# Optimization experiments

Measured on AMD Instinct MI355X. Metric: run time of the kernel, lower is better.

The kernel has to match this reference:

```python
import jax, jax.numpy as jnp
import numpy as np

BLOCK_SIZE = 64
NUM_STEPS = 3
# pad_type='post', init_type='ones', attention_mask=None


def setup_inputs() -> dict:
    key = jax.random.key(0)
    k1, k2, k3 = jax.random.split(key, 3)
    B, H, S, D = 4, 16, 4096, 64
    return {
        "query": jax.random.normal(k1, (B, H, S, D), dtype=jnp.float32),
        "key": jax.random.normal(k2, (B, H, S, D), dtype=jnp.float32),
        "value": jax.random.normal(k3, (B, H, S, D), dtype=jnp.float32),
    }


def _soba_monarch(query, key, value):
    B, H, S, D = query.shape
    bs = BLOCK_SIZE
    nb = -(-S // bs)                 # ceil(S / bs)
    pad = nb * bs - S                # post padding amount
    q = query / (D ** 0.5)

    pad_cfg = ((0, 0), (0, 0), (0, pad), (0, 0))
    Qb = jnp.pad(q, pad_cfg).reshape(B, H, nb, bs, D)      # (l j) v -> l j v
    Kb = jnp.pad(key, pad_cfg).reshape(B, H, nb, bs, D)    # (k i) v -> k i v

    # validity of positions in the padded sequence (post-pad)
    pos_valid = (jnp.arange(nb * bs) < S).reshape(nb, bs)  # [block, within]
    # left factor shape (..., j, l, k): rows of the flattened (l j) axis
    left_mask = jnp.broadcast_to(pos_valid.T[:, :, None], (bs, nb, nb))      # j l k
    # right factor shape (..., k, j, i): columns of the flattened (k i) axis
    right_mask = jnp.broadcast_to(pos_valid[:, None, :], (nb, bs, bs))       # k j i

    NEG = jnp.finfo(q.dtype).min
    # init_type = 'ones'
    left = jnp.broadcast_to(
        jnp.where(left_mask, 1.0 / nb, 0.0), (B, H, bs, nb, nb)
    ).astype(q.dtype)

    for _ in range(NUM_STEPS):
        # beta[k,j,i] = sum_{l,v} left[j,l,k] Q[l,j,v] K[k,i,v]
        beta = jnp.einsum('bhjlk,bhljv,bhkiv->bhkji', left, Qb, Kb, optimize=True)
        tau = jnp.swapaxes(jnp.sum(left, axis=-2), -1, -2)[..., None]        # bhkj1
        tau_zero = jnp.isclose(tau, 0.0)
        tau_safe = jnp.where(tau_zero, 1.0, tau)
        logits_r = jnp.where(right_mask & ~tau_zero, beta / tau_safe, NEG)
        right = jax.nn.softmax(logits_r, axis=-1)
        right = jnp.where(right_mask, right, 0.0)

        # alpha[j,1,k] = sum_i right[k,j,i] log right[k,j,i]  (xlogy)
        r_safe = jnp.where(right > 0, right, 1.0)
        alpha = jnp.sum(right * jnp.log(r_safe), axis=-1)                    # bhkj
        alpha = jnp.swapaxes(alpha, -1, -2)[..., None, :]                    # bhj1k

        beta2 = jnp.einsum('bhkji,bhljv,bhkiv->bhjlk', right, Qb, Kb, optimize=True)
        left = jax.nn.softmax(jnp.where(left_mask, beta2 - alpha, NEG), axis=-1)
        left = jnp.where(left_mask, left, 0.0)

    # multiply: z = L (R V)
    Vb = jnp.pad(value, pad_cfg).reshape(B, H, nb, bs, D)                    # k i v
    Y = jnp.einsum('bhkji,bhkiv->bhkjv', right, Vb)
    Z = jnp.einsum('bhjlk,bhkjv->bhljv', left, Y)
    z = Z.reshape(B, H, nb * bs, D)
    return z[..., :S, :]


def reference(query, key, value):
    return _soba_monarch(query, key, value)
```

## Files before the change

kernel.cpp:

```cpp
#include <hip/hip_runtime.h>


namespace {

typedef __attribute__((ext_vector_type(8))) short short8v;
typedef __attribute__((ext_vector_type(4))) float f32x4;

constexpr int HEADS = 64;
constexpr size_t HEADQ = 262144;
constexpr size_t MATF  = (size_t)HEADS * 262144;

#define MFMA(ACC, A, B) ACC = __builtin_amdgcn_mfma_f32_16x16x32_bf16(A, B, ACC, 0, 0, 0)
#define LD8(arr, row, g8) (*(const short8v*)((arr) + (row) * 72 + (g8) * 8))

__device__ __forceinline__ float rmax16(float m) {
    m = fmaxf(m, __shfl_xor(m, 1));
    m = fmaxf(m, __shfl_xor(m, 2));
    m = fmaxf(m, __shfl_xor(m, 4));
    m = fmaxf(m, __shfl_xor(m, 8));
    return m;
}
__device__ __forceinline__ float rsum16(float s) {
    s += __shfl_xor(s, 1);
    s += __shfl_xor(s, 2);
    s += __shfl_xor(s, 4);
    s += __shfl_xor(s, 8);
    return s;
}

__device__ __forceinline__ void bfsplit(float x, ushort& h, ushort& l) {
    uint u = __float_as_uint(x);
    uint hi = (u + 0x7FFFu + ((u >> 16) & 1u)) & 0xFFFF0000u;
    h = (ushort)(hi >> 16);
    l = (ushort)(__float_as_uint(x - __uint_as_float(hi)) >> 16);
}
__device__ __forceinline__ uint packbf(float x) {
    uint u = __float_as_uint(x);
    uint hi = (u + 0x7FFFu + ((u >> 16) & 1u)) & 0xFFFF0000u;
    return hi | (__float_as_uint(x - __uint_as_float(hi)) >> 16);
}

struct Frag16 { short8v h0, h1, l0, l1; };

__device__ __forceinline__ Frag16 split_load(const float* __restrict__ p, float s) {
    Frag16 f;
    #pragma unroll
    for (int q = 0; q < 4; ++q) {
        float4 a = *(const float4*)(p + 4 * q);
        float v[4] = {a.x * s, a.y * s, a.z * s, a.w * s};
        #pragma unroll
        for (int e = 0; e < 4; ++e) {
            ushort hh, ll; bfsplit(v[e], hh, ll);
            const int i = 4 * q + e;
            if (i < 8) { f.h0[i] = (short)hh; f.l0[i] = (short)ll; }
            else       { f.h1[i - 8] = (short)hh; f.l1[i - 8] = (short)ll; }
        }
    }
    return f;
}
__device__ __forceinline__ Frag16 unpack_load(const uint* __restrict__ p) {
    Frag16 f;
    #pragma unroll
    for (int q = 0; q < 2; ++q) {
        uint4 a = *(const uint4*)(p + 8 * q);
        uint4 b = *(const uint4*)(p + 8 * q + 4);
        uint vv[8] = {a.x, a.y, a.z, a.w, b.x, b.y, b.z, b.w};
        short8v h, l;
        #pragma unroll
        for (int e = 0; e < 8; ++e) {
            h[e] = (short)(vv[e] >> 16);
            l[e] = (short)(vv[e] & 0xFFFFu);
        }
        if (q == 0) { f.h0 = h; f.l0 = l; } else { f.h1 = h; f.l1 = l; }
    }
    return f;
}
__device__ __forceinline__ void store_rows(ushort* H, ushort* L, int r, int c0,
                                           const Frag16& f) {
    *(short8v*)(H + r * 72 + c0)     = f.h0;
    *(short8v*)(H + r * 72 + c0 + 8) = f.h1;
    *(short8v*)(L + r * 72 + c0)     = f.l0;
    *(short8v*)(L + r * 72 + c0 + 8) = f.l1;
}
__device__ __forceinline__ void scatter_tr(ushort* H, ushort* L, int r, int c0,
                                           const Frag16& f) {
    #pragma unroll
    for (int e = 0; e < 8; ++e) {
        H[(c0 + e) * 72 + r] = (ushort)f.h0[e];
        L[(c0 + e) * 72 + r] = (ushort)f.l0[e];
    }
    #pragma unroll
    for (int e = 0; e < 8; ++e) {
        H[(c0 + 8 + e) * 72 + r] = (ushort)f.h1[e];
        L[(c0 + 8 + e) * 72 + r] = (ushort)f.l1[e];
    }
}

__device__ __forceinline__ void mmstep(const ushort* AH, const ushort* AL,
                                       const ushort* BH, const ushort* BL,
                                       int w, int lo4, int hi4, f32x4 acc[4]) {
    #pragma unroll
    for (int ks = 0; ks < 2; ++ks) {
        short8v ah = LD8(AH, 16 * w + lo4, hi4 + 4 * ks);
        short8v al = LD8(AL, 16 * w + lo4, hi4 + 4 * ks);
        #pragma unroll
        for (int t = 0; t < 4; ++t) {
            short8v bh = LD8(BH, 16 * t + lo4, hi4 + 4 * ks);
            short8v bl = LD8(BL, 16 * t + lo4, hi4 + 4 * ks);
            MFMA(acc[t], ah, bh); MFMA(acc[t], ah, bl); MFMA(acc[t], al, bh);
        }
    }
}

__global__ __launch_bounds__(256) void kmean_kernel(const float* __restrict__ Q,
                                                    uint* __restrict__ M) {
    const int wg = blockIdx.x;
    const int h  = wg >> 4;
    const int j  = ((wg & 15) << 2) + (threadIdx.x >> 6);
    const int v  = threadIdx.x & 63;
    const float* base = Q + (size_t)h * HEADQ + (size_t)j * 64 + v;
    float acc = 0.f;
    #pragma unroll
    for (int l = 0; l < 64; ++l) acc += base[(size_t)l * 4096];
    M[((size_t)h * 64 + j) * 64 + v] = packbf(acc * (1.0f / 512.0f));
}

template<int FIRST, int LAST>
__global__ __launch_bounds__(256, 4) void bc_kernel(
    const uint*  __restrict__ Gsrc,
    const float* __restrict__ Kmat,
    const float* __restrict__ Vmat,
    const float* __restrict__ tauIn,
    uint*  __restrict__ HmOut,
    float* __restrict__ alphaOut,
    uint*  __restrict__ Yout)
{
    __shared__ __align__(16) ushort SM[18432];
    ushort* Ah = SM;          ushort* Al = SM + 4608;
    ushort* Bh = SM + 9216;   ushort* Bl = SM + 13824;

    const int wg = blockIdx.x, h = wg >> 6, k = wg & 63;
    const int tid = threadIdx.x, r = tid & 63, c0 = (tid >> 6) << 4;
    const int w = tid >> 6, lo4 = tid & 15, hi4 = (tid >> 4) & 3;

    {
        const uint* gp = FIRST ? Gsrc + ((size_t)h * 64 + r) * 64 + c0
                               : Gsrc + ((size_t)h * 64 + r) * 4096 + (size_t)k * 64 + c0;
        store_rows(Ah, Al, r, c0, unpack_load(gp));
    }
    Frag16 fk = split_load(Kmat + (size_t)h * HEADQ + (size_t)k * 4096 + r * 64 + c0, 1.f);
    store_rows(Bh, Bl, r, c0, fk);
    Frag16 fv;
    if (LAST)
        fv = split_load(Vmat + (size_t)h * HEADQ + (size_t)k * 4096 + r * 64 + c0, 1.f);
    float tvv[4];
    #pragma unroll
    for (int rr = 0; rr < 4; ++rr)
        tvv[rr] = FIRST ? 1.f : tauIn[((size_t)h * 64 + 16 * w + 4 * hi4 + rr) * 64 + k];
    __syncthreads();

    f32x4 acc[4] = {};
    mmstep(Ah, Al, Bh, Bl, w, lo4, hi4, acc);
    __syncthreads();

    #pragma unroll
    for (int rr = 0; rr < 4; ++rr) {
        const int j = 16 * w + 4 * hi4 + rr;
        const bool tz = !(tvv[rr] > 1e-8f);
        const float tvi = tz ? 1.f : 1.f / tvv[rr];
        float lg[4];
        #pragma unroll
        for (int t = 0; t < 4; ++t) lg[t] = acc[t][rr] * tvi;
        float m = rmax16(fmaxf(fmaxf(lg[0], lg[1]), fmaxf(lg[2], lg[3])));
        float e[4], s = 0.f;
        #pragma unroll
        for (int t = 0; t < 4; ++t) { e[t] = __expf(lg[t] - m); s += e[t]; }
        s = rsum16(s);
        const float inv = 1.f / s;
        float ap = 0.f;
        #pragma unroll
        for (int t = 0; t < 4; ++t) {
            const float rv = tz ? (1.f / 64.f) : e[t] * inv;
            ap += (rv > 0.f) ? rv * __logf(rv) : 0.f;
            ushort hh, ll; bfsplit(rv, hh, ll);
            Ah[j * 72 + 16 * t + lo4] = hh;
            Al[j * 72 + 16 * t + lo4] = ll;
        }
        ap = rsum16(ap);
        if (lo4 == 0) alphaOut[((size_t)h * 64 + k) * 64 + j] = ap;
    }
    scatter_tr(Bh, Bl, r, c0, fk);
    __syncthreads();

    f32x4 acc2[4] = {};
    mmstep(Ah, Al, Bh, Bl, w, lo4, hi4, acc2);
    f32x4 acc3[4] = {};
    if (LAST) {
        __syncthreads();
        scatter_tr(Bh, Bl, r, c0, fv);
        __syncthreads();
        mmstep(Ah, Al, Bh, Bl, w, lo4, hi4, acc3);
    }

    #pragma unroll
    for (int rr = 0; rr < 4; ++rr) {
        const int j = 16 * w + 4 * hi4 + rr;
        const size_t ob = ((size_t)h * 64 + k) * 4096 + (size_t)j * 64;
        #pragma unroll
        for (int t = 0; t < 4; ++t) {
            HmOut[ob + 16 * t + lo4] = packbf(acc2[t][rr]);
            if (LAST) Yout[ob + 16 * t + lo4] = packbf(acc3[t][rr]);
        }
    }
}

template<int LAST>
__global__ __launch_bounds__(256, 4) void da_kernel(
    const float* __restrict__ Q,
    const uint*  __restrict__ HmIn,
    const float* __restrict__ alphaIn,
    const uint*  __restrict__ Yin,
    uint*  __restrict__ Gout,
    float* __restrict__ tauOut,
    float* __restrict__ Zout)
{
    __shared__ __align__(16) ushort SM[18432];
    ushort* Ah = SM;          ushort* Al = SM + 4608;
    ushort* Bh = SM + 9216;   ushort* Bl = SM + 13824;

    const int wg = blockIdx.x, h = wg >> 6, j = wg & 63;
    const int tid = threadIdx.x, r = tid & 63, c0 = (tid >> 6) << 4;
    const int w = tid >> 6, lo4 = tid & 15, hi4 = (tid >> 4) & 3;

    Frag16 fq = split_load(Q + (size_t)h * HEADQ + (size_t)r * 4096 + (size_t)j * 64 + c0,
                           0.125f);
    store_rows(Ah, Al, r, c0, fq);
    {
        store_rows(Bh, Bl, r, c0,
                   unpack_load(HmIn + ((size_t)h * 64 + r) * 4096 + (size_t)j * 64 + c0));
    }
    Frag16 fy;
    if (LAST)
        fy = unpack_load(Yin + ((size_t)h * 64 + r) * 4096 + (size_t)j * 64 + c0);
    float av[4];
    #pragma unroll
    for (int t = 0; t < 4; ++t)
        av[t] = alphaIn[((size_t)h * 64 + 16 * t + lo4) * 64 + j];
    __syncthreads();

    f32x4 acc[4] = {};
    mmstep(Ah, Al, Bh, Bl, w, lo4, hi4, acc);
    __syncthreads();

    #pragma unroll
    for (int rr = 0; rr < 4; ++rr) {
        const int l = 16 * w + 4 * hi4 + rr;
        float lg[4];
        #pragma unroll
        for (int t = 0; t < 4; ++t) lg[t] = acc[t][rr] - av[t];
        float m = rmax16(fmaxf(fmaxf(lg[0], lg[1]), fmaxf(lg[2], lg[3])));
        float e[4], s = 0.f;
        #pragma unroll
        for (int t = 0; t < 4; ++t) { e[t] = __expf(lg[t] - m); s += e[t]; }
        s = rsum16(s);
        const float inv = 1.f / s;
        #pragma unroll
        for (int t = 0; t < 4; ++t) {
            const float lv = e[t] * inv;
            ushort hh, ll; bfsplit(lv, hh, ll);
            if (!LAST) { Bh[(16 * t + lo4) * 72 + l] = hh; Bl[(16 * t + lo4) * 72 + l] = ll; }
            else       { Bh[l * 72 + 16 * t + lo4] = hh; Bl[l * 72 + 16 * t + lo4] = ll; }
        }
    }
    if (!LAST) scatter_tr(Ah, Al, r, c0, fq);
    else       scatter_tr(Ah, Al, r, c0, fy);
    __syncthreads();

    if (!LAST) {
        f32x4 acc2[4] = {};
        f32x4 tacc = {};
        short8v onesb;
        #pragma unroll
        for (int e2 = 0; e2 < 8; ++e2) onesb[e2] = (lo4 == 0) ? (short)0x3F80 : (short)0;
        #pragma unroll
        for (int ks = 0; ks < 2; ++ks) {
            short8v ah = LD8(Bh, 16 * w + lo4, hi4 + 4 * ks);
            short8v al = LD8(Bl, 16 * w + lo4, hi4 + 4 * ks);
            MFMA(tacc, ah, onesb); MFMA(tacc, al, onesb);
            #pragma unroll
            for (int t = 0; t < 4; ++t) {
                short8v bh = LD8(Ah, 16 * t + lo4, hi4 + 4 * ks);
                short8v bl = LD8(Al, 16 * t + lo4, hi4 + 4 * ks);
                MFMA(acc2[t], ah, bh); MFMA(acc2[t], ah, bl); MFMA(acc2[t], al, bh);
            }
        }
        #pragma unroll
        for (int rr = 0; rr < 4; ++rr) {
            const int kq = 16 * w + 4 * hi4 + rr;
            if (lo4 == 0) tauOut[((size_t)h * 64 + j) * 64 + kq] = tacc[rr];
            const size_t gb = ((size_t)h * 64 + j) * 4096 + (size_t)kq * 64;
            #pragma unroll
            for (int t = 0; t < 4; ++t) Gout[gb + 16 * t + lo4] = packbf(acc2[t][rr]);
        }
    } else {
        f32x4 acc2[4] = {};
        #pragma unroll
        for (int ks = 0; ks < 2; ++ks) {
            short8v ah = LD8(Bh, 16 * w + lo4, hi4 + 4 * ks);
            short8v al = LD8(Bl, 16 * w + lo4, hi4 + 4 * ks);
            #pragma unroll
            for (int t = 0; t < 4; ++t) {
                short8v bh = LD8(Ah, 16 * t + lo4, hi4 + 4 * ks);
                short8v bl = LD8(Al, 16 * t + lo4, hi4 + 4 * ks);
                MFMA(acc2[t], ah, bh); MFMA(acc2[t], ah, bl); MFMA(acc2[t], al, bh);
            }
        }
        #pragma unroll
        for (int rr = 0; rr < 4; ++rr) {
            const int l = 16 * w + 4 * hi4 + rr;
            const size_t zb = (size_t)h * HEADQ + (size_t)l * 4096 + (size_t)j * 64;
            #pragma unroll
            for (int t = 0; t < 4; ++t) Zout[zb + 16 * t + lo4] = acc2[t][rr];
        }
    }
}

}

extern "C" void kernel_launch(void* const* d_in, const int* in_sizes, int n_in,
                              void* d_out, int out_size, void* d_ws, size_t ws_size,
                              hipStream_t stream) {
    const float* Q = (const float*)d_in[0];
    const float* K = (const float*)d_in[1];
    const float* V = (const float*)d_in[2];
    float* out = (float*)d_out;

    char* ws = (char*)d_ws;
    const size_t MB = 1024 * 1024;
    uint*  G   = (uint*)(ws);
    uint*  Hm  = (uint*)(ws + 64 * MB);
    uint*  M   = (uint*)(ws + 128 * MB);
    float* al  = (float*)(ws + 129 * MB);
    float* tau = (float*)(ws + 130 * MB);

    const bool bigws = ws_size >= (size_t)195 * MB;
    uint*  Ybuf = bigws ? (uint*)(ws + 131 * MB) : (uint*)out;
    float* Zdst = bigws ? out : (float*)G;

    dim3 blk(256), grid(HEADS * 64);

    kmean_kernel<<<dim3(1024), blk, 0, stream>>>(Q, M);
    bc_kernel<1, 0><<<grid, blk, 0, stream>>>(M, K, nullptr, nullptr, Hm, al, nullptr);
    da_kernel<0>   <<<grid, blk, 0, stream>>>(Q, Hm, al, nullptr, G, tau, nullptr);
    bc_kernel<0, 0><<<grid, blk, 0, stream>>>(G, K, nullptr, tau, Hm, al, nullptr);
    da_kernel<0>   <<<grid, blk, 0, stream>>>(Q, Hm, al, nullptr, G, tau, nullptr);
    bc_kernel<0, 1><<<grid, blk, 0, stream>>>(G, K, V, tau, Hm, al, Ybuf);
    da_kernel<1>   <<<grid, blk, 0, stream>>>(Q, Hm, al, Ybuf, nullptr, nullptr, Zdst);
    if (!bigws)
        hipMemcpyAsync(d_out, Zdst, MATF * sizeof(float), hipMemcpyDeviceToDevice, stream);
}
```

Before: 328.9 us.

## Process two blocks per workgroup with register prefetch of next block's inputs

Both bc and da kernels now handle two consecutive k/j blocks per workgroup, halving the grid. While computing the current block, they prefetch the next block's raw G/K/tau or Q/Hm/alpha data into registers so global latency overlaps the MFMA work. The alpha and tau buffers are transposed so per-block reads become contiguous. The trade-offs are fewer workgroups in flight, more registers, and extra barriers per iteration.

```diff
diff --git a/kernel.cpp b/kernel.cpp
--- a/kernel.cpp
+++ b/kernel.cpp
@@ -40,38 +40,42 @@
     return hi | (__float_as_uint(x - __uint_as_float(hi)) >> 16);
 }
 
+struct RawU  { uint4 a, b, c, d; };
+struct RawF  { float4 a, b, c, d; };
 struct Frag16 { short8v h0, h1, l0, l1; };
 
-__device__ __forceinline__ Frag16 split_load(const float* __restrict__ p, float s) {
+__device__ __forceinline__ RawU loadU(const uint* __restrict__ p) {
+    RawU r;
+    r.a = *(const uint4*)(p);      r.b = *(const uint4*)(p + 4);
+    r.c = *(const uint4*)(p + 8);  r.d = *(const uint4*)(p + 12);
+    return r;
+}
+__device__ __forceinline__ RawF loadF(const float* __restrict__ p) {
+    RawF r;
+    r.a = *(const float4*)(p);     r.b = *(const float4*)(p + 4);
+    r.c = *(const float4*)(p + 8); r.d = *(const float4*)(p + 12);
+    return r;
+}
+__device__ __forceinline__ Frag16 unpackR(const RawU& r) {
+    uint vv[16] = {r.a.x, r.a.y, r.a.z, r.a.w, r.b.x, r.b.y, r.b.z, r.b.w,
+                   r.c.x, r.c.y, r.c.z, r.c.w, r.d.x, r.d.y, r.d.z, r.d.w};
     Frag16 f;
     #pragma unroll
-    for (int q = 0; q < 4; ++q) {
-        float4 a = *(const float4*)(p + 4 * q);
-        float v[4] = {a.x * s, a.y * s, a.z * s, a.w * s};
-        #pragma unroll
-        for (int e = 0; e < 4; ++e) {
-            ushort hh, ll; bfsplit(v[e], hh, ll);
-            const int i = 4 * q + e;
-            if (i < 8) { f.h0[i] = (short)hh; f.l0[i] = (short)ll; }
-            else       { f.h1[i - 8] = (short)hh; f.l1[i - 8] = (short)ll; }
-        }
+    for (int e = 0; e < 8; ++e) {
+        f.h0[e] = (short)(vv[e] >> 16);      f.l0[e] = (short)(vv[e] & 0xFFFFu);
+        f.h1[e] = (short)(vv[e + 8] >> 16);  f.l1[e] = (short)(vv[e + 8] & 0xFFFFu);
     }
     return f;
 }
-__device__ __forceinline__ Frag16 unpack_load(const uint* __restrict__ p) {
+__device__ __forceinline__ Frag16 splitR(const RawF& r, float s) {
+    float vv[16] = {r.a.x*s, r.a.y*s, r.a.z*s, r.a.w*s, r.b.x*s, r.b.y*s, r.b.z*s, r.b.w*s,
+                    r.c.x*s, r.c.y*s, r.c.z*s, r.c.w*s, r.d.x*s, r.d.y*s, r.d.z*s, r.d.w*s};
     Frag16 f;
     #pragma unroll
-    for (int q = 0; q < 2; ++q) {
-        uint4 a = *(const uint4*)(p + 8 * q);
-        uint4 b = *(const uint4*)(p + 8 * q + 4);
-        uint vv[8] = {a.x, a.y, a.z, a.w, b.x, b.y, b.z, b.w};
-        short8v h, l;
-        #pragma unroll
-        for (int e = 0; e < 8; ++e) {
-            h[e] = (short)(vv[e] >> 16);
-            l[e] = (short)(vv[e] & 0xFFFFu);
-        }
-        if (q == 0) { f.h0 = h; f.l0 = l; } else { f.h1 = h; f.l1 = l; }
+    for (int e = 0; e < 16; ++e) {
+        ushort hh, ll; bfsplit(vv[e], hh, ll);
+        if (e < 8) { f.h0[e] = (short)hh; f.l0[e] = (short)ll; }
+        else       { f.h1[e - 8] = (short)hh; f.l1[e - 8] = (short)ll; }
     }
     return f;
 }
@@ -139,78 +143,109 @@
     ushort* Ah = SM;          ushort* Al = SM + 4608;
     ushort* Bh = SM + 9216;   ushort* Bl = SM + 13824;
 
-    const int wg = blockIdx.x, h = wg >> 6, k = wg & 63;
+    const int wg = blockIdx.x, h = wg >> 5, k0 = (wg & 31) << 1;
     const int tid = threadIdx.x, r = tid & 63, c0 = (tid >> 6) << 4;
     const int w = tid >> 6, lo4 = tid & 15, hi4 = (tid >> 4) & 3;
 
-    {
-        const uint* gp = FIRST ? Gsrc + ((size_t)h * 64 + r) * 64 + c0
-                               : Gsrc + ((size_t)h * 64 + r) * 4096 + (size_t)k * 64 + c0;
-        store_rows(Ah, Al, r, c0, unpack_load(gp));
-    }
-    Frag16 fk = split_load(Kmat + (size_t)h * HEADQ + (size_t)k * 4096 + r * 64 + c0, 1.f);
-    store_rows(Bh, Bl, r, c0, fk);
-    Frag16 fv;
-    if (LAST)
-        fv = split_load(Vmat + (size_t)h * HEADQ + (size_t)k * 4096 + r * 64 + c0, 1.f);
-    float tvv[4];
-    #pragma unroll
-    for (int rr = 0; rr < 4; ++rr)
-        tvv[rr] = FIRST ? 1.f : tauIn[((size_t)h * 64 + 16 * w + 4 * hi4 + rr) * 64 + k];
-    __syncthreads();
-
-    f32x4 acc[4] = {};
-    mmstep(Ah, Al, Bh, Bl, w, lo4, hi4, acc);
-    __syncthreads();
-
-    #pragma unroll
-    for (int rr = 0; rr < 4; ++rr) {
-        const int j = 16 * w + 4 * hi4 + rr;
-        const bool tz = !(tvv[rr] > 1e-8f);
-        const float tvi = tz ? 1.f : 1.f / tvv[rr];
-        float lg[4];
+    const uint*  gB = Gsrc + (FIRST ? ((size_t)h * 64 + r) * 64 + c0
+                                    : ((size_t)h * 64 + r) * 4096 + c0);
+    const float* kB = Kmat + (size_t)h * HEADQ + (size_t)r * 64 + c0;
+
+    RawU gcur = loadU(FIRST ? gB : gB + (size_t)k0 * 64);
+    RawF kcur = loadF(kB + (size_t)k0 * 4096);
+    float tcur0, tcur1, tcur2, tcur3;
+    if (!FIRST) {
+        const float* tp = tauIn + ((size_t)h * 64 + k0) * 64 + 16 * w + 4 * hi4;
+        tcur0 = tp[0]; tcur1 = tp[1]; tcur2 = tp[2]; tcur3 = tp[3];
+    } else { tcur0 = tcur1 = tcur2 = tcur3 = 1.f; }
+
+    #pragma unroll
+    for (int t = 0; t < 2; ++t) {
+        const int k = k0 + t;
+
+        store_rows(Ah, Al, r, c0, unpackR(gcur));
+        Frag16 fk = splitR(kcur, 1.f);
+        store_rows(Bh, Bl, r, c0, fk);
+
+        RawU gnext; RawF knext;
+        float tn0 = 1.f, tn1 = 1.f, tn2 = 1.f, tn3 = 1.f;
+        if (t == 0) {
+            gnext = loadU(FIRST ? gB : gB + (size_t)(k + 1) * 64);
+            knext = loadF(kB + (size_t)(k + 1) * 4096);
+            if (!FIRST) {
+                const float* tp = tauIn + ((size_t)h * 64 + k + 1) * 64 + 16 * w + 4 * hi4;
+                tn0 = tp[0]; tn1 = tp[1]; tn2 = tp[2]; tn3 = tp[3];
+            }
+        }
+        __syncthreads();
+
+        f32x4 acc[4] = {};
+        mmstep(Ah, Al, Bh, Bl, w, lo4, hi4, acc);
+        __syncthreads();
+
+        RawF vraw;
+        if (LAST)
+            vraw = loadF(Vmat + (size_t)h * HEADQ + (size_t)k * 4096 + r * 64 + c0);
+
+        const float tvv[4] = {tcur0, tcur1, tcur2, tcur3};
         #pragma unroll
-        for (int t = 0; t < 4; ++t) lg[t] = acc[t][rr] * tvi;
-        float m = rmax16(fmaxf(fmaxf(lg[0], lg[1]), fmaxf(lg[2], lg[3])));
-        float e[4], s = 0.f;
+        for (int rr = 0; rr < 4; ++rr) {
+            const int j = 16 * w + 4 * hi4 + rr;
+            const bool tz = !(tvv[rr] > 1e-8f);
+            const float tvi = tz ? 1.f : 1.f / tvv[rr];
+            float lg[4];
+            #pragma unroll
+            for (int tt = 0; tt < 4; ++tt) lg[tt] = acc[tt][rr] * tvi;
+            float m = rmax16(fmaxf(fmaxf(lg[0], lg[1]), fmaxf(lg[2], lg[3])));
+            float e[4], s = 0.f;
+            #pragma unroll
+            for (int tt = 0; tt < 4; ++tt) { e[tt] = __expf(lg[tt] - m); s += e[tt]; }
+            s = rsum16(s);
+            const float inv = 1.f / s;
+            float ap = 0.f;
+            #pragma unroll
+            for (int tt = 0; tt < 4; ++tt) {
+                const float rv = tz ? (1.f / 64.f) : e[tt] * inv;
+                ap += (rv > 0.f) ? rv * __logf(rv) : 0.f;
+                ushort hh, ll; bfsplit(rv, hh, ll);
+                Ah[j * 72 + 16 * tt + lo4] = hh;
+                Al[j * 72 + 16 * tt + lo4] = ll;
+            }
+            ap = rsum16(ap);
+            if (lo4 == 0) alphaOut[((size_t)h * 64 + j) * 64 + k] = ap;
+        }
+        scatter_tr(Bh, Bl, r, c0, fk);
+        __syncthreads();
+
+        f32x4 acc2[4] = {};
+        mmstep(Ah, Al, Bh, Bl, w, lo4, hi4, acc2);
         #pragma unroll
-        for (int t = 0; t < 4; ++t) { e[t] = __expf(lg[t] - m); s += e[t]; }
-        s = rsum16(s);
-        const float inv = 1.f / s;
-        float ap = 0.f;
-        #pragma unroll
-        for (int t = 0; t < 4; ++t) {
-            const float rv = tz ? (1.f / 64.f) : e[t] * inv;
-            ap += (rv > 0.f) ? rv * __logf(rv) : 0.f;
-            ushort hh, ll; bfsplit(rv, hh, ll);
-            Ah[j * 72 + 16 * t + lo4] = hh;
-            Al[j * 72 + 16 * t + lo4] = ll;
-        }
-        ap = rsum16(ap);
-        if (lo4 == 0) alphaOut[((size_t)h * 64 + k) * 64 + j] = ap;
-    }
-    scatter_tr(Bh, Bl, r, c0, fk);
-    __syncthreads();
-
-    f32x4 acc2[4] = {};
-    mmstep(Ah, Al, Bh, Bl, w, lo4, hi4, acc2);
-    f32x4 acc3[4] = {};
-    if (LAST) {
-        __syncthreads();
-        scatter_tr(Bh, Bl, r, c0, fv);
-        __syncthreads();
-        mmstep(Ah, Al, Bh, Bl, w, lo4, hi4, acc3);
-    }
-
-    #pragma unroll
-    for (int rr = 0; rr < 4; ++rr) {
-        const int j = 16 * w + 4 * hi4 + rr;
-        const size_t ob = ((size_t)h * 64 + k) * 4096 + (size_t)j * 64;
-        #pragma unroll
-        for (int t = 0; t < 4; ++t) {
-            HmOut[ob + 16 * t + lo4] = packbf(acc2[t][rr]);
-            if (LAST) Yout[ob + 16 * t + lo4] = packbf(acc3[t][rr]);
-        }
+        for (int rr = 0; rr < 4; ++rr) {
+            const int j = 16 * w + 4 * hi4 + rr;
+            const size_t ob = ((size_t)h * 64 + k) * 4096 + (size_t)j * 64;
+            #pragma unroll
+            for (int tt = 0; tt < 4; ++tt)
+                HmOut[ob + 16 * tt + lo4] = packbf(acc2[tt][rr]);
+        }
+        if (LAST) {
+            __syncthreads();
+            scatter_tr(Bh, Bl, r, c0, splitR(vraw, 1.f));
+            __syncthreads();
+            f32x4 acc3[4] = {};
+            mmstep(Ah, Al, Bh, Bl, w, lo4, hi4, acc3);
+            #pragma unroll
+            for (int rr = 0; rr < 4; ++rr) {
+                const int j = 16 * w + 4 * hi4 + rr;
+                const size_t ob = ((size_t)h * 64 + k) * 4096 + (size_t)j * 64;
+                #pragma unroll
+                for (int tt = 0; tt < 4; ++tt)
+                    Yout[ob + 16 * tt + lo4] = packbf(acc3[tt][rr]);
+            }
+        }
+        __syncthreads();
+
+        gcur = gnext; kcur = knext;
+        tcur0 = tn0; tcur1 = tn1; tcur2 = tn2; tcur3 = tn3;
     }
 }
 
@@ -228,100 +263,123 @@
     ushort* Ah = SM;          ushort* Al = SM + 4608;
     ushort* Bh = SM + 9216;   ushort* Bl = SM + 13824;
 
-    const int wg = blockIdx.x, h = wg >> 6, j = wg & 63;
+    const int wg = blockIdx.x, h = wg >> 5, j0 = (wg & 31) << 1;
     const int tid = threadIdx.x, r = tid & 63, c0 = (tid >> 6) << 4;
     const int w = tid >> 6, lo4 = tid & 15, hi4 = (tid >> 4) & 3;
 
-    Frag16 fq = split_load(Q + (size_t)h * HEADQ + (size_t)r * 4096 + (size_t)j * 64 + c0,
-                           0.125f);
-    store_rows(Ah, Al, r, c0, fq);
+    const float* qB = Q    + (size_t)h * HEADQ + (size_t)r * 4096 + c0;
+    const uint*  hB = HmIn + ((size_t)h * 64 + r) * 4096 + c0;
+
+    RawF qcur = loadF(qB + (size_t)j0 * 64);
+    RawU hcur = loadU(hB + (size_t)j0 * 64);
+    float acur0, acur1, acur2, acur3;
     {
-        store_rows(Bh, Bl, r, c0,
-                   unpack_load(HmIn + ((size_t)h * 64 + r) * 4096 + (size_t)j * 64 + c0));
-    }
-    Frag16 fy;
-    if (LAST)
-        fy = unpack_load(Yin + ((size_t)h * 64 + r) * 4096 + (size_t)j * 64 + c0);
-    float av[4];
-    #pragma unroll
-    for (int t = 0; t < 4; ++t)
-        av[t] = alphaIn[((size_t)h * 64 + 16 * t + lo4) * 64 + j];
-    __syncthreads();
-
-    f32x4 acc[4] = {};
-    mmstep(Ah, Al, Bh, Bl, w, lo4, hi4, acc);
-    __syncthreads();
-
-    #pragma unroll
-    for (int rr = 0; rr < 4; ++rr) {
-        const int l = 16 * w + 4 * hi4 + rr;
-        float lg[4];
-        #pragma unroll
-        for (int t = 0; t < 4; ++t) lg[t] = acc[t][rr] - av[t];
-        float m = rmax16(fmaxf(fmaxf(lg[0], lg[1]), fmaxf(lg[2], lg[3])));
-        float e[4], s = 0.f;
-        #pragma unroll
-        for (int t = 0; t < 4; ++t) { e[t] = __expf(lg[t] - m); s += e[t]; }
-        s = rsum16(s);
-        const float inv = 1.f / s;
-        #pragma unroll
-        for (int t = 0; t < 4; ++t) {
-            const float lv = e[t] * inv;
-            ushort hh, ll; bfsplit(lv, hh, ll);
-            if (!LAST) { Bh[(16 * t + lo4) * 72 + l] = hh; Bl[(16 * t + lo4) * 72 + l] = ll; }
-            else       { Bh[l * 72 + 16 * t + lo4] = hh; Bl[l * 72 + 16 * t + lo4] = ll; }
-        }
-    }
-    if (!LAST) scatter_tr(Ah, Al, r, c0, fq);
-    else       scatter_tr(Ah, Al, r, c0, fy);
-    __syncthreads();
-
-    if (!LAST) {
-        f32x4 acc2[4] = {};
-        f32x4 tacc = {};
-        short8v onesb;
-        #pragma unroll
-        for (int e2 = 0; e2 < 8; ++e2) onesb[e2] = (lo4 == 0) ? (short)0x3F80 : (short)0;
-        #pragma unroll
-        for (int ks = 0; ks < 2; ++ks) {
-            short8v ah = LD8(Bh, 16 * w + lo4, hi4 + 4 * ks);
-            short8v al = LD8(Bl, 16 * w + lo4, hi4 + 4 * ks);
-            MFMA(tacc, ah, onesb); MFMA(tacc, al, onesb);
-            #pragma unroll
-            for (int t = 0; t < 4; ++t) {
-                short8v bh = LD8(Ah, 16 * t + lo4, hi4 + 4 * ks);
-                short8v bl = LD8(Al, 16 * t + lo4, hi4 + 4 * ks);
-                MFMA(acc2[t], ah, bh); MFMA(acc2[t], ah, bl); MFMA(acc2[t], al, bh);
-            }
-        }
-        #pragma unroll
-        for (int rr = 0; rr < 4; ++rr) {
-            const int kq = 16 * w + 4 * hi4 + rr;
-            if (lo4 == 0) tauOut[((size_t)h * 64 + j) * 64 + kq] = tacc[rr];
-            const size_t gb = ((size_t)h * 64 + j) * 4096 + (size_t)kq * 64;
-            #pragma unroll
-            for (int t = 0; t < 4; ++t) Gout[gb + 16 * t + lo4] = packbf(acc2[t][rr]);
-        }
-    } else {
-        f32x4 acc2[4] = {};
-        #pragma unroll
-        for (int ks = 0; ks < 2; ++ks) {
-            short8v ah = LD8(Bh, 16 * w + lo4, hi4 + 4 * ks);
-            short8v al = LD8(Bl, 16 * w + lo4, hi4 + 4 * ks);
-            #pragma unroll
-            for (int t = 0; t < 4; ++t) {
-                short8v bh = LD8(Ah, 16 * t + lo4, hi4 + 4 * ks);
-                short8v bl = LD8(Al, 16 * t + lo4, hi4 + 4 * ks);
-                MFMA(acc2[t], ah, bh); MFMA(acc2[t], ah, bl); MFMA(acc2[t], al, bh);
-            }
-        }
+        const float* ap = alphaIn + ((size_t)h * 64 + j0) * 64;
+        acur0 = ap[lo4]; acur1 = ap[16 + lo4]; acur2 = ap[32 + lo4]; acur3 = ap[48 + lo4];
+    }
+
+    #pragma unroll
+    for (int t = 0; t < 2; ++t) {
+        const int j = j0 + t;
+
+        Frag16 fq = splitR(qcur, 0.125f);
+        store_rows(Ah, Al, r, c0, fq);
+        store_rows(Bh, Bl, r, c0, unpackR(hcur));
+
+        RawF qnext; RawU hnext;
+        float an0 = 0.f, an1 = 0.f, an2 = 0.f, an3 = 0.f;
+        if (t == 0) {
+            qnext = loadF(qB + (size_t)(j + 1) * 64);
+            hnext = loadU(hB + (size_t)(j + 1) * 64);
+            const float* ap = alphaIn + ((size_t)h * 64 + j + 1) * 64;
+            an0 = ap[lo4]; an1 = ap[16 + lo4]; an2 = ap[32 + lo4]; an3 = ap[48 + lo4];
+        }
+        __syncthreads();
+
+        f32x4 acc[4] = {};
+        mmstep(Ah, Al, Bh, Bl, w, lo4, hi4, acc);
+        __syncthreads();
+
+        RawU yraw;
+        if (LAST)
+            yraw = loadU(Yin + ((size_t)h * 64 + r) * 4096 + (size_t)j * 64 + c0);
+
+        const float av[4] = {acur0, acur1, acur2, acur3};
         #pragma unroll
         for (int rr = 0; rr < 4; ++rr) {
             const int l = 16 * w + 4 * hi4 + rr;
-            const size_t zb = (size_t)h * HEADQ + (size_t)l * 4096 + (size_t)j * 64;
-            #pragma unroll
-            for (int t = 0; t < 4; ++t) Zout[zb + 16 * t + lo4] = acc2[t][rr];
-        }
+            float lg[4];
+            #pragma unroll
+            for (int tt = 0; tt < 4; ++tt) lg[tt] = acc[tt][rr] - av[tt];
+            float m = rmax16(fmaxf(fmaxf(lg[0], lg[1]), fmaxf(lg[2], lg[3])));
+            float e[4], s = 0.f;
+            #pragma unroll
+            for (int tt = 0; tt < 4; ++tt) { e[tt] = __expf(lg[tt] - m); s += e[tt]; }
+            s = rsum16(s);
+            const float inv = 1.f / s;
+            #pragma unroll
+            for (int tt = 0; tt < 4; ++tt) {
+                const float lv = e[tt] * inv;
+                ushort hh, ll; bfsplit(lv, hh, ll);
+                if (!LAST) { Bh[(16 * tt + lo4) * 72 + l] = hh; Bl[(16 * tt + lo4) * 72 + l] = ll; }
+                else       { Bh[l * 72 + 16 * tt + lo4] = hh; Bl[l * 72 + 16 * tt + lo4] = ll; }
+            }
+        }
+        if (!LAST) scatter_tr(Ah, Al, r, c0, fq);
+        else       scatter_tr(Ah, Al, r, c0, unpackR(yraw));
+        __syncthreads();
+
+        if (!LAST) {
+            f32x4 acc2[4] = {};
+            f32x4 tacc = {};
+            short8v onesb;
+            #pragma unroll
+            for (int e2 = 0; e2 < 8; ++e2) onesb[e2] = (lo4 == 0) ? (short)0x3F80 : (short)0;
+            #pragma unroll
+            for (int ks = 0; ks < 2; ++ks) {
+                short8v ah = LD8(Bh, 16 * w + lo4, hi4 + 4 * ks);
+                short8v al = LD8(Bl, 16 * w + lo4, hi4 + 4 * ks);
+                MFMA(tacc, ah, onesb); MFMA(tacc, al, onesb);
+                #pragma unroll
+                for (int tt = 0; tt < 4; ++tt) {
+                    short8v bh = LD8(Ah, 16 * tt + lo4, hi4 + 4 * ks);
+                    short8v bl = LD8(Al, 16 * tt + lo4, hi4 + 4 * ks);
+                    MFMA(acc2[tt], ah, bh); MFMA(acc2[tt], ah, bl); MFMA(acc2[tt], al, bh);
+                }
+            }
+            #pragma unroll
+            for (int rr = 0; rr < 4; ++rr) {
+                const int kq = 16 * w + 4 * hi4 + rr;
+                if (lo4 == 0) tauOut[((size_t)h * 64 + kq) * 64 + j] = tacc[rr];
+                const size_t gb = ((size_t)h * 64 + j) * 4096 + (size_t)kq * 64;
+                #pragma unroll
+                for (int tt = 0; tt < 4; ++tt) Gout[gb + 16 * tt + lo4] = packbf(acc2[tt][rr]);
+            }
+        } else {
+            f32x4 acc2[4] = {};
+            #pragma unroll
+            for (int ks = 0; ks < 2; ++ks) {
+                short8v ah = LD8(Bh, 16 * w + lo4, hi4 + 4 * ks);
+                short8v al = LD8(Bl, 16 * w + lo4, hi4 + 4 * ks);
+                #pragma unroll
+                for (int tt = 0; tt < 4; ++tt) {
+                    short8v bh = LD8(Ah, 16 * tt + lo4, hi4 + 4 * ks);
+                    short8v bl = LD8(Al, 16 * tt + lo4, hi4 + 4 * ks);
+                    MFMA(acc2[tt], ah, bh); MFMA(acc2[tt], ah, bl); MFMA(acc2[tt], al, bh);
+                }
+            }
+            #pragma unroll
+            for (int rr = 0; rr < 4; ++rr) {
+                const int l = 16 * w + 4 * hi4 + rr;
+                const size_t zb = (size_t)h * HEADQ + (size_t)l * 4096 + (size_t)j * 64;
+                #pragma unroll
+                for (int tt = 0; tt < 4; ++tt) Zout[zb + 16 * tt + lo4] = acc2[tt][rr];
+            }
+        }
+        __syncthreads();
+
+        qcur = qnext; hcur = hnext;
+        acur0 = an0; acur1 = an1; acur2 = an2; acur3 = an3;
     }
 }
 
@@ -347,7 +405,7 @@
     uint*  Ybuf = bigws ? (uint*)(ws + 131 * MB) : (uint*)out;
     float* Zdst = bigws ? out : (float*)G;
 
-    dim3 blk(256), grid(HEADS * 64);
+    dim3 blk(256), grid(2048);
 
     kmean_kernel<<<dim3(1024), blk, 0, stream>>>(Q, M);
     bc_kernel<1, 0><<<grid, blk, 0, stream>>>(M, K, nullptr, nullptr, Hm, al, nullptr);
```

Measured after the change: 355.1 us. 1.08x slower.
